# Optimization experiments

Hardware: AMD Instinct MI355X
Metric: run time of the kernel (lower is better)

The kernel has to match this reference:

```python
import jax, jax.numpy as jnp
import numpy as np

STATE_DIM = 1024
ACTION_DIM = 512
TASK_DIM = 64
EMBED = 64
HID = 128
B = 256


def setup_inputs() -> dict:
    key = jax.random.key(0)
    ks = jax.random.split(key, 24)
    s = 0.02
    inp = {
        "obs": jax.random.normal(ks[0], (B, STATE_DIM), dtype=jnp.float32),
        "task_label": jax.random.normal(ks[1], (B, TASK_DIM), dtype=jnp.float32),
        "action": jax.random.randint(ks[2], (B,), 0, ACTION_DIM, dtype=jnp.int64 if jax.config.jax_enable_x64 else jnp.int32),
        # task encoder: Linear(64,64) ReLU Linear(64,64) ReLU
        "we1": jax.random.normal(ks[3], (TASK_DIM, EMBED)) * s,
        "be1": jnp.zeros((EMBED,), jnp.float32),
        "we2": jax.random.normal(ks[4], (EMBED, EMBED)) * s,
        "be2": jnp.zeros((EMBED,), jnp.float32),
        # h_action net_W: Linear(64,128) ReLU Linear(128, 512*1024)
        "aw1": jax.random.normal(ks[5], (EMBED, HID)) * s,
        "aw1b": jnp.zeros((HID,), jnp.float32),
        "aw2": jax.random.normal(ks[6], (HID, ACTION_DIM * STATE_DIM)) * s,
        "aw2b": jnp.zeros((ACTION_DIM * STATE_DIM,), jnp.float32),
        # h_action net_b: Linear(64,128) ReLU Linear(128, 512)
        "ab1": jax.random.normal(ks[7], (EMBED, HID)) * s,
        "ab1b": jnp.zeros((HID,), jnp.float32),
        "ab2": jax.random.normal(ks[8], (HID, ACTION_DIM)) * s,
        "ab2b": jnp.zeros((ACTION_DIM,), jnp.float32),
        # h_critic net_W: Linear(64,128) ReLU Linear(128, 1*1024)
        "cw1": jax.random.normal(ks[9], (EMBED, HID)) * s,
        "cw1b": jnp.zeros((HID,), jnp.float32),
        "cw2": jax.random.normal(ks[10], (HID, 1 * STATE_DIM)) * s,
        "cw2b": jnp.zeros((STATE_DIM,), jnp.float32),
        # h_critic net_b: Linear(64,128) ReLU Linear(128, 1)
        "cb1": jax.random.normal(ks[11], (EMBED, HID)) * s,
        "cb1b": jnp.zeros((HID,), jnp.float32),
        "cb2": jax.random.normal(ks[12], (HID, 1)) * s,
        "cb2b": jnp.zeros((1,), jnp.float32),
    }
    return inp


def reference(obs, task_label, action, we1, be1, we2, be2,
              aw1, aw1b, aw2, aw2b, ab1, ab1b, ab2, ab2b,
              cw1, cw1b, cw2, cw2b, cb1, cb1b, cb2, cb2b):
    relu = jax.nn.relu
    b = obs.shape[0]
    # DummyBody: phi = phi_a = phi_v = obs
    # task encoder -> z [B, EMBED]
    z = relu(relu(task_label @ we1 + be1) @ we2 + be2)
    # hypernet-generated actor head: W [B, A, S], b [B, A]
    Wa = (relu(z @ aw1 + aw1b) @ aw2 + aw2b).reshape(b, ACTION_DIM, STATE_DIM)
    ba = relu(z @ ab1 + ab1b) @ ab2 + ab2b
    # hypernet-generated critic head: W [B, 1, S], b [B, 1]
    Wv = (relu(z @ cw1 + cw1b) @ cw2 + cw2b).reshape(b, 1, STATE_DIM)
    bv = relu(z @ cb1 + cb1b) @ cb2 + cb2b
    # bmm apply (torch.bmm(W, phi.unsqueeze(-1)).squeeze(-1) + b)
    logits = jnp.einsum('boi,bi->bo', Wa, obs) + ba
    v = jnp.einsum('boi,bi->bo', Wv, obs) + bv
    logp = jax.nn.log_softmax(logits, axis=-1)
    log_prob = jnp.take_along_axis(logp, action[:, None].astype(jnp.int32), axis=-1)  # [B,1]
    entropy = -jnp.sum(jnp.exp(logp) * logp, axis=-1, keepdims=True)  # [B,1]
    return logits, action, log_prob, entropy, v
```

## Files before the change

kernel.cpp:

```cpp
#include <hip/hip_runtime.h>
#include <hip/hip_bf16.h>

#define B_SZ 256
#define SDIM 1024
#define ADIM 512

#define BK 32
#define BM 256
#define BN 160
#define PAD 36
#define NSTEPS (SDIM / BK)

typedef __attribute__((ext_vector_type(8))) short bf16x8;
typedef __attribute__((ext_vector_type(4))) short bf16x4;
typedef __attribute__((ext_vector_type(4))) float f32x4;

__device__ __forceinline__ unsigned short f2bf(float x) {
  union { float f; unsigned u; } v; v.f = x;
  unsigned r = v.u + 0x7FFFu + ((v.u >> 16) & 1u);
  return (unsigned short)(r >> 16);
}

__global__ __launch_bounds__(128) void kprep(
    const float* __restrict__ task, const int* __restrict__ action,
    const float* __restrict__ we1, const float* __restrict__ be1,
    const float* __restrict__ we2, const float* __restrict__ be2,
    const float* __restrict__ aw1, const float* __restrict__ aw1b,
    const float* __restrict__ ab1, const float* __restrict__ ab1b,
    const float* __restrict__ ab2, const float* __restrict__ ab2b,
    const float* __restrict__ cw1, const float* __restrict__ cw1b,
    const float* __restrict__ cb1, const float* __restrict__ cb1b,
    const float* __restrict__ cb2, const float* __restrict__ cb2b,
    float* __restrict__ ws_ha, float* __restrict__ ws_hc,
    float* __restrict__ out)
{
  const int b = blockIdx.x, t = threadIdx.x;
  __shared__ float s_task[64], s_t1[64], s_z[64], s_hb[128], s_red[128];

  if (t < 64) s_task[t] = task[b * 64 + t];
  __syncthreads();
  if (t < 64) {
    float a = be1[t];
    for (int e = 0; e < 64; ++e) a += s_task[e] * we1[e * 64 + t];
    s_t1[t] = fmaxf(a, 0.0f);
  }
  __syncthreads();
  if (t < 64) {
    float a = be2[t];
    for (int e = 0; e < 64; ++e) a += s_t1[e] * we2[e * 64 + t];
    s_z[t] = fmaxf(a, 0.0f);
  }
  __syncthreads();
  {
    float a1 = aw1b[t], a2 = ab1b[t], a3 = cw1b[t], a4 = cb1b[t];
    for (int e = 0; e < 64; ++e) {
      const float zv = s_z[e];
      a1 += zv * aw1[e * 128 + t];
      a2 += zv * ab1[e * 128 + t];
      a3 += zv * cw1[e * 128 + t];
      a4 += zv * cb1[e * 128 + t];
    }
    ws_ha[b * 128 + t] = fmaxf(a1, 0.0f);
    s_hb[t] = fmaxf(a2, 0.0f);
    ws_hc[b * 128 + t] = fmaxf(a3, 0.0f);
    s_red[t] = fmaxf(a4, 0.0f) * cb2[t];
  }
  __syncthreads();
  for (int o = t; o < ADIM; o += 128) {
    float a = ab2b[o];
    for (int h = 0; h < 128; ++h) a += s_hb[h] * ab2[h * ADIM + o];
    out[b * ADIM + o] = a;
  }
  for (int s = 64; s > 0; s >>= 1) {
    __syncthreads();
    if (t < s) s_red[t] += s_red[t + s];
  }
  if (t == 0) {
    out[131840 + b] = s_red[0] + cb2b[0];
    out[131072 + b] = (float)action[b];
  }
}

__global__ __launch_bounds__(512) void khyper(
    const float* __restrict__ obs,
    const float* __restrict__ aw2, const float* __restrict__ aw2b,
    const float* __restrict__ cw2, const float* __restrict__ cw2b,
    const float* __restrict__ ws_ha, const float* __restrict__ ws_hc,
    float* __restrict__ d_out)
{
  __shared__ unsigned short A_lds[2][BM][PAD];
  __shared__ unsigned short B_lds[2][BN][PAD];
  __shared__ float logits_buf[BM];

  const int tid = threadIdx.x;
  const int blk = blockIdx.x;
  const bool critic = (blk >= ADIM);
  const int o = critic ? 0 : blk;
  const float* Wmat = critic ? cw2 : aw2;
  const long wstride = critic ? (long)SDIM : (long)ADIM * SDIM;
  const float* bias_row = (critic ? cw2b : aw2b) + (long)o * SDIM;
  const float* haW = critic ? ws_hc : ws_ha;

  const float* aptr[4];
  int aoff[4];
#pragma unroll
  for (int i = 0; i < 4; ++i) {
    const int idx = tid + i * 512;
    const int row = idx >> 3, c4 = idx & 7;
    aptr[i] = obs + (long)row * SDIM + c4 * 4;
    aoff[i] = row * PAD + c4 * 4;
  }
  const float* bptr[3];
  int boff[3];
#pragma unroll
  for (int i = 0; i < 3; ++i) {
    const int idx = tid + i * 512;
    const int row = idx >> 3, c4 = idx & 7;
    if (row < 128) bptr[i] = Wmat + (long)row * wstride + (long)o * SDIM + c4 * 4;
    else           bptr[i] = bias_row + c4 * 4;
    boff[i] = row * PAD + c4 * 4;
  }

  const int lane = tid & 63;
  const int wv = tid >> 6;
  const int mbase = (wv & 3) * 64;
  const int nbase = (wv >> 2) * 80;
  const int lrow = lane & 15;
  const int lk = (lane >> 4) * 8;

  f32x4 acc[4][5];
#pragma unroll
  for (int mf = 0; mf < 4; ++mf)
#pragma unroll
    for (int nf = 0; nf < 5; ++nf) acc[mf][nf] = (f32x4)(0.0f);

  float4 aR[4]; float4 bR[3];

  auto load_step = [&](int t) {
    const int k0 = t * BK;
#pragma unroll
    for (int i = 0; i < 4; ++i) aR[i] = *(const float4*)(aptr[i] + k0);
#pragma unroll
    for (int i = 0; i < 2; ++i) bR[i] = *(const float4*)(bptr[i] + k0);
    if (tid < 256) bR[2] = *(const float4*)(bptr[2] + k0);
  };

  auto store_step = [&](int buf) {
    unsigned short* Ab = &A_lds[buf][0][0];
    unsigned short* Bb = &B_lds[buf][0][0];
#pragma unroll
    for (int i = 0; i < 4; ++i) {
      ushort4 p; p.x = f2bf(aR[i].x); p.y = f2bf(aR[i].y); p.z = f2bf(aR[i].z); p.w = f2bf(aR[i].w);
      *(ushort4*)(Ab + aoff[i]) = p;
    }
#pragma unroll
    for (int i = 0; i < 2; ++i) {
      ushort4 p; p.x = f2bf(bR[i].x); p.y = f2bf(bR[i].y); p.z = f2bf(bR[i].z); p.w = f2bf(bR[i].w);
      *(ushort4*)(Bb + boff[i]) = p;
    }
    if (tid < 256) {
      ushort4 p; p.x = f2bf(bR[2].x); p.y = f2bf(bR[2].y); p.z = f2bf(bR[2].z); p.w = f2bf(bR[2].w);
      *(ushort4*)(Bb + boff[2]) = p;
    }
  };

  auto compute_step = [&](int buf) {
    const unsigned short* Ab = &A_lds[buf][0][0];
    const unsigned short* Bb = &B_lds[buf][0][0];
    union U8 { bf16x8 v8; bf16x4 v4[2]; };
    bf16x8 af[4]; bf16x8 bfr[5];
#pragma unroll
    for (int mf = 0; mf < 4; ++mf) {
      const unsigned short* p = Ab + (mbase + mf * 16 + lrow) * PAD + lk;
      U8 u; u.v4[0] = *(const bf16x4*)p; u.v4[1] = *(const bf16x4*)(p + 4);
      af[mf] = u.v8;
    }
#pragma unroll
    for (int nf = 0; nf < 5; ++nf) {
      const unsigned short* p = Bb + (nbase + nf * 16 + lrow) * PAD + lk;
      U8 u; u.v4[0] = *(const bf16x4*)p; u.v4[1] = *(const bf16x4*)(p + 4);
      bfr[nf] = u.v8;
    }
#pragma unroll
    for (int mf = 0; mf < 4; ++mf)
#pragma unroll
      for (int nf = 0; nf < 5; ++nf)
        acc[mf][nf] = __builtin_amdgcn_mfma_f32_16x16x32_bf16(af[mf], bfr[nf], acc[mf][nf], 0, 0, 0);
  };

  load_step(0);
  store_step(0);
  __syncthreads();
  int cur = 0;
#pragma unroll 2
  for (int t = 0; t < NSTEPS; ++t) {
    if (t + 1 < NSTEPS) load_step(t + 1);
    compute_step(cur);
    if (t + 1 < NSTEPS) store_step(cur ^ 1);
    __syncthreads();
    cur ^= 1;
  }

  if (tid < BM) logits_buf[tid] = 0.0f;
  __syncthreads();

  float val[4][4];
#pragma unroll
  for (int mf = 0; mf < 4; ++mf)
#pragma unroll
    for (int r = 0; r < 4; ++r) val[mf][r] = 0.0f;

#pragma unroll
  for (int nf = 0; nf < 5; ++nf) {
    const int hidx = nbase + nf * 16 + lrow;
    if (hidx < 128) {
#pragma unroll
      for (int mf = 0; mf < 4; ++mf) {
        const int m0 = mbase + mf * 16 + ((lane >> 4) << 2);
#pragma unroll
        for (int r = 0; r < 4; ++r)
          val[mf][r] += haW[(m0 + r) * 128 + hidx] * acc[mf][nf][r];
      }
    } else if (hidx == 128) {
#pragma unroll
      for (int mf = 0; mf < 4; ++mf)
#pragma unroll
        for (int r = 0; r < 4; ++r) val[mf][r] += acc[mf][nf][r];
    }
  }

#pragma unroll
  for (int mf = 0; mf < 4; ++mf)
#pragma unroll
    for (int r = 0; r < 4; ++r) {
      float v = val[mf][r];
      v += __shfl_xor(v, 1, 64);
      v += __shfl_xor(v, 2, 64);
      v += __shfl_xor(v, 4, 64);
      v += __shfl_xor(v, 8, 64);
      val[mf][r] = v;
    }
  if ((lane & 15) == 0) {
#pragma unroll
    for (int mf = 0; mf < 4; ++mf)
#pragma unroll
      for (int r = 0; r < 4; ++r)
        atomicAdd(&logits_buf[mbase + mf * 16 + ((lane >> 4) << 2) + r], val[mf][r]);
  }
  __syncthreads();

  if (tid < BM) {
    if (!critic) {
      float* p = d_out + (long)tid * ADIM + o;
      *p += logits_buf[tid];
    } else {
      d_out[131840 + tid] += logits_buf[tid];
    }
  }
}

__global__ __launch_bounds__(256) void kfinal(const int* __restrict__ action,
                                              float* __restrict__ d_out)
{
  const int b = blockIdx.x, t = threadIdx.x;
  const float* lrow = d_out + (long)b * ADIM;
  __shared__ float sM[4], sS[4], sT[4];

  const float x0 = lrow[t], x1 = lrow[t + 256];
  float m = fmaxf(x0, x1);
#pragma unroll
  for (int s = 1; s < 64; s <<= 1) m = fmaxf(m, __shfl_xor(m, s, 64));
  const int wv = t >> 6, ln = t & 63;
  if (ln == 0) sM[wv] = m;
  __syncthreads();
  m = fmaxf(fmaxf(sM[0], sM[1]), fmaxf(sM[2], sM[3]));

  const float d0 = x0 - m, d1 = x1 - m;
  const float e0 = expf(d0), e1 = expf(d1);
  float s1 = e0 + e1;
  float s2 = e0 * d0 + e1 * d1;
#pragma unroll
  for (int s = 1; s < 64; s <<= 1) {
    s1 += __shfl_xor(s1, s, 64);
    s2 += __shfl_xor(s2, s, 64);
  }
  if (ln == 0) { sS[wv] = s1; sT[wv] = s2; }
  __syncthreads();
  if (t == 0) {
    const float S = sS[0] + sS[1] + sS[2] + sS[3];
    const float T = sT[0] + sT[1] + sT[2] + sT[3];
    const float lnS = logf(S);
    const int a = action[b];
    d_out[131328 + b] = (lrow[a] - m) - lnS;
    d_out[131584 + b] = lnS - T / S;
  }
}

extern "C" void kernel_launch(void* const* d_in, const int* in_sizes, int n_in,
                              void* d_out_v, int out_size, void* d_ws, size_t ws_size,
                              hipStream_t stream) {
  const float* obs   = (const float*)d_in[0];
  const float* task  = (const float*)d_in[1];
  const int*   action= (const int*)  d_in[2];
  const float* we1   = (const float*)d_in[3];
  const float* be1   = (const float*)d_in[4];
  const float* we2   = (const float*)d_in[5];
  const float* be2   = (const float*)d_in[6];
  const float* aw1   = (const float*)d_in[7];
  const float* aw1b  = (const float*)d_in[8];
  const float* aw2   = (const float*)d_in[9];
  const float* aw2b  = (const float*)d_in[10];
  const float* ab1   = (const float*)d_in[11];
  const float* ab1b  = (const float*)d_in[12];
  const float* ab2   = (const float*)d_in[13];
  const float* ab2b  = (const float*)d_in[14];
  const float* cw1   = (const float*)d_in[15];
  const float* cw1b  = (const float*)d_in[16];
  const float* cw2   = (const float*)d_in[17];
  const float* cw2b  = (const float*)d_in[18];
  const float* cb1   = (const float*)d_in[19];
  const float* cb1b  = (const float*)d_in[20];
  const float* cb2   = (const float*)d_in[21];
  const float* cb2b  = (const float*)d_in[22];
  float* out = (float*)d_out_v;
  float* ws_ha = (float*)d_ws;
  float* ws_hc = ws_ha + 256 * 128;

  kprep<<<256, 128, 0, stream>>>(task, action, we1, be1, we2, be2, aw1, aw1b,
                                 ab1, ab1b, ab2, ab2b, cw1, cw1b, cb1, cb1b,
                                 cb2, cb2b, ws_ha, ws_hc, out);
  khyper<<<513, 512, 0, stream>>>(obs, aw2, aw2b, cw2, cw2b, ws_ha, ws_hc, out);
  kfinal<<<256, 256, 0, stream>>>(action, out);
}
```

Before: 180.4 us.

## Pre-convert obs to bf16 and feed MFMA directly from global, dropping LDS staging

The prep kernel now converts obs to bf16 once into workspace. The hypernet GEMM kernel no longer stages A and B tiles through double-buffered LDS. Each lane loads its MFMA fragments straight from global memory, with the weight loads register double-buffered and converted in registers. This removes LDS traffic, the per-step barriers and the repeated obs conversion across 513 blocks. The cost is that A fragments are re-read from L2 per wave rather than shared, and the block ordering is changed so the critic runs first.

```diff
diff --git a/kernel.cpp b/kernel.cpp
--- a/kernel.cpp
+++ b/kernel.cpp
@@ -6,13 +6,9 @@
 #define ADIM 512
 
 #define BK 32
-#define BM 256
-#define BN 160
-#define PAD 36
 #define NSTEPS (SDIM / BK)
 
 typedef __attribute__((ext_vector_type(8))) short bf16x8;
-typedef __attribute__((ext_vector_type(4))) short bf16x4;
 typedef __attribute__((ext_vector_type(4))) float f32x4;
 
 __device__ __forceinline__ unsigned short f2bf(float x) {
@@ -22,6 +18,7 @@
 }
 
 __global__ __launch_bounds__(128) void kprep(
+    const float* __restrict__ obs,
     const float* __restrict__ task, const int* __restrict__ action,
     const float* __restrict__ we1, const float* __restrict__ be1,
     const float* __restrict__ we2, const float* __restrict__ be2,
@@ -32,10 +29,24 @@
     const float* __restrict__ cb1, const float* __restrict__ cb1b,
     const float* __restrict__ cb2, const float* __restrict__ cb2b,
     float* __restrict__ ws_ha, float* __restrict__ ws_hc,
+    unsigned short* __restrict__ ws_obs,
     float* __restrict__ out)
 {
   const int b = blockIdx.x, t = threadIdx.x;
   __shared__ float s_task[64], s_t1[64], s_z[64], s_hb[128], s_red[128];
+
+  {
+    const float4* orow = (const float4*)(obs + (size_t)b * SDIM);
+    ushort4* wrow = (ushort4*)(ws_obs + (size_t)b * SDIM);
+#pragma unroll
+    for (int i = 0; i < 2; ++i) {
+      const int idx = t + i * 128;
+      float4 v = orow[idx];
+      ushort4 u;
+      u.x = f2bf(v.x); u.y = f2bf(v.y); u.z = f2bf(v.z); u.w = f2bf(v.w);
+      wrow[idx] = u;
+    }
+  }
 
   if (t < 64) s_task[t] = task[b * 64 + t];
   __syncthreads();
@@ -81,52 +92,44 @@
   }
 }
 
-__global__ __launch_bounds__(512) void khyper(
-    const float* __restrict__ obs,
+__global__ __launch_bounds__(512, 2) void khyper(
+    const unsigned short* __restrict__ ws_obs,
     const float* __restrict__ aw2, const float* __restrict__ aw2b,
     const float* __restrict__ cw2, const float* __restrict__ cw2b,
     const float* __restrict__ ws_ha, const float* __restrict__ ws_hc,
     float* __restrict__ d_out)
 {
-  __shared__ unsigned short A_lds[2][BM][PAD];
-  __shared__ unsigned short B_lds[2][BN][PAD];
-  __shared__ float logits_buf[BM];
+  __shared__ float logits_buf[B_SZ];
 
   const int tid = threadIdx.x;
   const int blk = blockIdx.x;
-  const bool critic = (blk >= ADIM);
-  const int o = critic ? 0 : blk;
-  const float* Wmat = critic ? cw2 : aw2;
-  const long wstride = critic ? (long)SDIM : (long)ADIM * SDIM;
-  const float* bias_row = (critic ? cw2b : aw2b) + (long)o * SDIM;
+  const bool critic = (blk == 0);
+  const int o = critic ? 0 : (blk - 1);
   const float* haW = critic ? ws_hc : ws_ha;
-
-  const float* aptr[4];
-  int aoff[4];
-#pragma unroll
-  for (int i = 0; i < 4; ++i) {
-    const int idx = tid + i * 512;
-    const int row = idx >> 3, c4 = idx & 7;
-    aptr[i] = obs + (long)row * SDIM + c4 * 4;
-    aoff[i] = row * PAD + c4 * 4;
-  }
-  const float* bptr[3];
-  int boff[3];
-#pragma unroll
-  for (int i = 0; i < 3; ++i) {
-    const int idx = tid + i * 512;
-    const int row = idx >> 3, c4 = idx & 7;
-    if (row < 128) bptr[i] = Wmat + (long)row * wstride + (long)o * SDIM + c4 * 4;
-    else           bptr[i] = bias_row + c4 * 4;
-    boff[i] = row * PAD + c4 * 4;
-  }
 
   const int lane = tid & 63;
   const int wv = tid >> 6;
   const int mbase = (wv & 3) * 64;
   const int nbase = (wv >> 2) * 80;
   const int lrow = lane & 15;
-  const int lk = (lane >> 4) * 8;
+  const int lk8 = (lane >> 4) * 8;
+
+  const unsigned short* pA[4];
+#pragma unroll
+  for (int mf = 0; mf < 4; ++mf) {
+    const int rowm = mbase + mf * 16 + lrow;
+    pA[mf] = ws_obs + (size_t)rowm * SDIM + lk8;
+  }
+  const float* pB[5];
+#pragma unroll
+  for (int nf = 0; nf < 5; ++nf) {
+    const int h = nbase + nf * 16 + lrow;
+    const float* base;
+    if (critic) base = (h < 128) ? (cw2 + (size_t)h * SDIM) : cw2b;
+    else        base = (h < 128) ? (aw2 + (size_t)h * (ADIM * SDIM) + (size_t)o * SDIM)
+                                 : (aw2b + (size_t)o * SDIM);
+    pB[nf] = base + lk8;
+  }
 
   f32x4 acc[4][5];
 #pragma unroll
@@ -134,74 +137,53 @@
 #pragma unroll
     for (int nf = 0; nf < 5; ++nf) acc[mf][nf] = (f32x4)(0.0f);
 
-  float4 aR[4]; float4 bR[3];
-
-  auto load_step = [&](int t) {
-    const int k0 = t * BK;
-#pragma unroll
-    for (int i = 0; i < 4; ++i) aR[i] = *(const float4*)(aptr[i] + k0);
-#pragma unroll
-    for (int i = 0; i < 2; ++i) bR[i] = *(const float4*)(bptr[i] + k0);
-    if (tid < 256) bR[2] = *(const float4*)(bptr[2] + k0);
-  };
-
-  auto store_step = [&](int buf) {
-    unsigned short* Ab = &A_lds[buf][0][0];
-    unsigned short* Bb = &B_lds[buf][0][0];
-#pragma unroll
-    for (int i = 0; i < 4; ++i) {
-      ushort4 p; p.x = f2bf(aR[i].x); p.y = f2bf(aR[i].y); p.z = f2bf(aR[i].z); p.w = f2bf(aR[i].w);
-      *(ushort4*)(Ab + aoff[i]) = p;
-    }
-#pragma unroll
-    for (int i = 0; i < 2; ++i) {
-      ushort4 p; p.x = f2bf(bR[i].x); p.y = f2bf(bR[i].y); p.z = f2bf(bR[i].z); p.w = f2bf(bR[i].w);
-      *(ushort4*)(Bb + boff[i]) = p;
-    }
-    if (tid < 256) {
-      ushort4 p; p.x = f2bf(bR[2].x); p.y = f2bf(bR[2].y); p.z = f2bf(bR[2].z); p.w = f2bf(bR[2].w);
-      *(ushort4*)(Bb + boff[2]) = p;
-    }
-  };
-
-  auto compute_step = [&](int buf) {
-    const unsigned short* Ab = &A_lds[buf][0][0];
-    const unsigned short* Bb = &B_lds[buf][0][0];
-    union U8 { bf16x8 v8; bf16x4 v4[2]; };
-    bf16x8 af[4]; bf16x8 bfr[5];
-#pragma unroll
-    for (int mf = 0; mf < 4; ++mf) {
-      const unsigned short* p = Ab + (mbase + mf * 16 + lrow) * PAD + lk;
-      U8 u; u.v4[0] = *(const bf16x4*)p; u.v4[1] = *(const bf16x4*)(p + 4);
-      af[mf] = u.v8;
-    }
-#pragma unroll
-    for (int nf = 0; nf < 5; ++nf) {
-      const unsigned short* p = Bb + (nbase + nf * 16 + lrow) * PAD + lk;
-      U8 u; u.v4[0] = *(const bf16x4*)p; u.v4[1] = *(const bf16x4*)(p + 4);
-      bfr[nf] = u.v8;
-    }
-#pragma unroll
-    for (int mf = 0; mf < 4; ++mf)
-#pragma unroll
-      for (int nf = 0; nf < 5; ++nf)
-        acc[mf][nf] = __builtin_amdgcn_mfma_f32_16x16x32_bf16(af[mf], bfr[nf], acc[mf][nf], 0, 0, 0);
-  };
-
-  load_step(0);
-  store_step(0);
-  __syncthreads();
-  int cur = 0;
-#pragma unroll 2
-  for (int t = 0; t < NSTEPS; ++t) {
-    if (t + 1 < NSTEPS) load_step(t + 1);
-    compute_step(cur);
-    if (t + 1 < NSTEPS) store_step(cur ^ 1);
-    __syncthreads();
-    cur ^= 1;
-  }
-
-  if (tid < BM) logits_buf[tid] = 0.0f;
+#define LOADB(BUF, T)                                                   \
+  {                                                                     \
+    const size_t k0_ = (size_t)(T) * BK;                                \
+    _Pragma("unroll")                                                   \
+    for (int nf = 0; nf < 5; ++nf) {                                    \
+      BUF[nf][0] = *(const float4*)(pB[nf] + k0_);                      \
+      BUF[nf][1] = *(const float4*)(pB[nf] + k0_ + 4);                  \
+    }                                                                   \
+  }
+
+#define COMPUTE(BUF, T)                                                 \
+  {                                                                     \
+    const size_t k0_ = (size_t)(T) * BK;                                \
+    bf16x8 af[4];                                                       \
+    _Pragma("unroll")                                                   \
+    for (int mf = 0; mf < 4; ++mf)                                      \
+      af[mf] = *(const bf16x8*)(pA[mf] + k0_);                          \
+    bf16x8 bfr[5];                                                      \
+    _Pragma("unroll")                                                   \
+    for (int nf = 0; nf < 5; ++nf) {                                    \
+      bf16x8 v;                                                         \
+      v[0] = (short)f2bf(BUF[nf][0].x); v[1] = (short)f2bf(BUF[nf][0].y); \
+      v[2] = (short)f2bf(BUF[nf][0].z); v[3] = (short)f2bf(BUF[nf][0].w); \
+      v[4] = (short)f2bf(BUF[nf][1].x); v[5] = (short)f2bf(BUF[nf][1].y); \
+      v[6] = (short)f2bf(BUF[nf][1].z); v[7] = (short)f2bf(BUF[nf][1].w); \
+      bfr[nf] = v;                                                      \
+    }                                                                   \
+    _Pragma("unroll")                                                   \
+    for (int mf = 0; mf < 4; ++mf)                                      \
+      _Pragma("unroll")                                                 \
+      for (int nf = 0; nf < 5; ++nf)                                    \
+        acc[mf][nf] = __builtin_amdgcn_mfma_f32_16x16x32_bf16(af[mf], bfr[nf], acc[mf][nf], 0, 0, 0); \
+  }
+
+  float4 b0[5][2], b1[5][2];
+  LOADB(b0, 0);
+#pragma unroll 1
+  for (int t = 0; t < NSTEPS; t += 2) {
+    LOADB(b1, t + 1);
+    COMPUTE(b0, t);
+    if (t + 2 < NSTEPS) LOADB(b0, t + 2);
+    COMPUTE(b1, t + 1);
+  }
+#undef LOADB
+#undef COMPUTE
+
+  if (tid < B_SZ) logits_buf[tid] = 0.0f;
   __syncthreads();
 
   float val[4][4];
@@ -249,9 +231,9 @@
   }
   __syncthreads();
 
-  if (tid < BM) {
+  if (tid < B_SZ) {
     if (!critic) {
-      float* p = d_out + (long)tid * ADIM + o;
+      float* p = d_out + (size_t)tid * ADIM + o;
       *p += logits_buf[tid];
     } else {
       d_out[131840 + tid] += logits_buf[tid];
@@ -263,7 +245,7 @@
                                               float* __restrict__ d_out)
 {
   const int b = blockIdx.x, t = threadIdx.x;
-  const float* lrow = d_out + (long)b * ADIM;
+  const float* lrow = d_out + (size_t)b * ADIM;
   __shared__ float sM[4], sS[4], sT[4];
 
   const float x0 = lrow[t], x1 = lrow[t + 256];
@@ -325,10 +307,11 @@
   float* out = (float*)d_out_v;
   float* ws_ha = (float*)d_ws;
   float* ws_hc = ws_ha + 256 * 128;
-
-  kprep<<<256, 128, 0, stream>>>(task, action, we1, be1, we2, be2, aw1, aw1b,
+  unsigned short* ws_obs = (unsigned short*)(ws_hc + 256 * 128);
+
+  kprep<<<256, 128, 0, stream>>>(obs, task, action, we1, be1, we2, be2, aw1, aw1b,
                                  ab1, ab1b, ab2, ab2b, cw1, cw1b, cb1, cb1b,
-                                 cb2, cb2b, ws_ha, ws_hc, out);
-  khyper<<<513, 512, 0, stream>>>(obs, aw2, aw2b, cw2, cw2b, ws_ha, ws_hc, out);
+                                 cb2, cb2b, ws_ha, ws_hc, ws_obs, out);
+  khyper<<<513, 512, 0, stream>>>(ws_obs, aw2, aw2b, cw2, cw2b, ws_ha, ws_hc, out);
   kfinal<<<256, 256, 0, stream>>>(action, out);
 }
```

After: 344.3 us. 1.91x slower.
